# Performance work log

Hardware: AMD Instinct MI355X
Metric: run time of the kernel (lower is better)

The kernel has to match this reference:

```python
import jax, jax.numpy as jnp
import numpy as np

WS, OWS, HEADS, DIM = 16, 24, 6, 192
PAD = (OWS - WS) // 2
NQ, NKV = WS * WS, OWS * OWS
TABLE = (WS + OWS - 1) ** 2


def _rpi():
    # replicates WindowsHandling.get_relative_position_index_for_overlap_window
    c = np.arange(WS)
    ori = np.stack(np.meshgrid(c, c, indexing='ij')).reshape(2, -1)
    e = np.arange(OWS)
    ext = np.stack(np.meshgrid(e, e, indexing='ij')).reshape(2, -1)
    rc = (ext[:, None, :] - ori[:, :, None]).transpose(1, 2, 0).astype(np.int64)
    rc[..., 0] += WS - OWS + 1
    rc[..., 1] += WS - OWS + 1
    rc[..., 0] *= WS + OWS - 1
    # mod mimics torch's negative advanced-index wraparound into the table
    return (rc.sum(-1) % TABLE).astype(np.int32)  # (NQ, NKV)


def _extract_patches(xp, nh, nw):
    # torch.nn.Unfold(kernel=OWS, stride=WS) equivalent on NHWC input.
    # xp: (b, PH, PW, c) -> (b*nh*nw, OWS*OWS, c), row-major window order.
    b, PH, PW, c = xp.shape
    i = (np.arange(nh) * WS)[:, None] + np.arange(OWS)[None, :]
    j = (np.arange(nw) * WS)[:, None] + np.arange(OWS)[None, :]
    t = jnp.take(xp, jnp.asarray(i.reshape(-1)), axis=1).reshape(b, nh, OWS, PW, c)
    t = jnp.take(t, jnp.asarray(j.reshape(-1)), axis=3).reshape(b, nh, OWS, nw, OWS, c)
    return t.transpose(0, 1, 3, 2, 4, 5).reshape(b * nh * nw, OWS * OWS, c)


def _attn_mask(h, w):
    # shift_size == 0 branch of get_attention_mask_for_overlap_window:
    # kv positions falling into the zero padding get -100.
    vm = np.zeros((1, h + 2 * PAD, w + 2 * PAD, 1), np.float32)
    vm[:, PAD:-PAD, PAD:-PAD, :] = 1.0
    nh, nw = h // WS, w // WS
    kv = np.asarray(_extract_patches(jnp.asarray(vm), nh, nw)).reshape(nh * nw, NKV)
    m = np.where(kv[:, None, :] > 0, 0.0, -100.0).astype(np.float32)
    return np.broadcast_to(m, (nh * nw, NQ, NKV)).copy()


def setup_inputs():
    key = jax.random.key(0)
    ks = jax.random.split(key, 8)
    b, h, w = 2, 160, 160
    s = 0.02
    return {
        'x': jax.random.normal(ks[0], (b, h, w, DIM), jnp.float32),
        'rpi': jnp.asarray(_rpi()),
        'attn_mask': jnp.asarray(_attn_mask(h, w)),
        'q_w': jax.random.normal(ks[1], (DIM, DIM), jnp.float32) * s,
        'q_b': jnp.zeros((DIM,), jnp.float32),
        'kv_w': jax.random.normal(ks[2], (DIM, 2 * DIM), jnp.float32) * s,
        'kv_b': jnp.zeros((2 * DIM,), jnp.float32),
        'bias_table': jax.random.normal(ks[3], (TABLE, HEADS), jnp.float32) * s,
        'gating_w': jax.random.normal(ks[4], (DIM, DIM), jnp.float32) * s,
        'gating_b': jnp.ones((DIM,), jnp.float32),
        'proj_w': jax.random.normal(ks[5], (DIM, DIM), jnp.float32) * s,
        'proj_b': jnp.zeros((DIM,), jnp.float32),
    }


def reference(x, rpi, attn_mask, q_w, q_b, kv_w, kv_b, bias_table, gating_w, gating_b, proj_w, proj_b):
    b, h, w, c = x.shape
    d = c // HEADS
    scale = d ** -0.5
    nh, nw = h // WS, w // WS
    nwin = nh * nw
    # shift_size == 0 path: zero-pad for overlapping kv windows
    x_pad = jnp.pad(x, ((0, 0), (PAD, PAD), (PAD, PAD), (0, 0)))
    # q windows (non-overlapping window partition)
    xw = x.reshape(b, nh, WS, nw, WS, c).transpose(0, 1, 3, 2, 4, 5).reshape(b * nwin, NQ, c)
    # kv windows (overlapping, Unfold equivalent)
    xpw = _extract_patches(x_pad, nh, nw)  # (b*nwin, NKV, c)
    gates = xw @ gating_w + gating_b                       # (b*nwin, NQ, c)
    q = (xw @ q_w + q_b).reshape(-1, NQ, HEADS, d).transpose(0, 2, 1, 3) * scale
    kv = xpw @ kv_w + kv_b
    k = kv[..., :c].reshape(-1, NKV, HEADS, d).transpose(0, 2, 1, 3)
    v = kv[..., c:].reshape(-1, NKV, HEADS, d).transpose(0, 2, 1, 3)
    attn = jnp.einsum('bhqd,bhkd->bhqk', q, k)             # (b*nwin, H, NQ, NKV)
    bias = bias_table[rpi.reshape(-1)].reshape(NQ, NKV, HEADS).transpose(2, 0, 1)
    attn = attn + bias[None]
    attn = attn.reshape(b, nwin, HEADS, NQ, NKV) + attn_mask[None, :, None]
    attn = jax.nn.softmax(attn, axis=-1).reshape(b * nwin, HEADS, NQ, NKV)
    out = jnp.einsum('bhqk,bhkd->bhqd', attn, v).transpose(0, 2, 1, 3).reshape(-1, NQ, c)
    out = out * gates
    out = out.reshape(b, nh, nw, WS, WS, c).transpose(0, 1, 3, 2, 4, 5).reshape(b, h, w, c)
    return out @ proj_w + proj_b
```

## Files before the change

### kernel.cpp

```cpp
#include <hip/hip_runtime.h>
#include <hip/hip_bf16.h>
#include <stdint.h>

typedef __bf16 bf16x8  __attribute__((ext_vector_type(8)));
typedef __bf16 bf16x4  __attribute__((ext_vector_type(4)));
typedef __bf16 bf16x16 __attribute__((ext_vector_type(16)));
typedef float  f32x4   __attribute__((ext_vector_type(4)));
typedef float  f32x16  __attribute__((ext_vector_type(16)));
typedef uint32_t u32;

#define MFMA16(a, b, c) __builtin_amdgcn_mfma_f32_16x16x32_bf16((a), (b), (c), 0, 0, 0)
#define MFMA32(a, b, c) __builtin_amdgcn_mfma_f32_32x32x16_bf16((a), (b), (c), 0, 0, 0)

#if __has_builtin(__builtin_amdgcn_exp2f)
#define EXP2F(x) __builtin_amdgcn_exp2f(x)
#else
#define EXP2F(x) exp2f(x)
#endif

constexpr int CH = 160, CW = 160, CC = 192, CHEADS = 6, CD = 32;
constexpr int CNQ = 256, CNKV = 576, CPH = 168;
constexpr float LOG2E = 1.44269504088896340736f;
constexpr float QSCALE_L2E = 0.17677669529663687f * 1.44269504088896340736f;

__global__ __launch_bounds__(256)
void prep_k(const int* __restrict__ rpi, const float* __restrict__ tab,
            const float* __restrict__ q_w, const float* __restrict__ g_w,
            const float* __restrict__ kv_w, const float* __restrict__ p_w,
            const float* __restrict__ q_b, const float* __restrict__ g_b,
            const float* __restrict__ kv_b, const float* __restrict__ p_b,
            __bf16* __restrict__ BTh, u32* __restrict__ mt,
            __bf16* __restrict__ Wt, __bf16* __restrict__ Wp,
            float* __restrict__ b768, float* __restrict__ pb,
            __bf16* __restrict__ KVb)
{
    const int bidg = blockIdx.x;
    if (bidg < 216) {
        int idx = bidg * 256 + threadIdx.x;
        int lane = idx & 63;
        int rest = idx >> 6;
        int ktg = rest % 18; rest /= 18;
        int qtg = rest & 7;
        int head = rest >> 3;
        int l31 = lane & 31, hi = lane >> 5;
        int q = qtg * 32 + l31;
        bf16x16 o16;
#pragma unroll
        for (int g = 0; g < 4; ++g) {
            int4 ri = *(const int4*)(rpi + q * CNKV + ktg * 32 + 4 * hi + g * 8);
            o16[g * 4 + 0] = (__bf16)(tab[ri.x * CHEADS + head] * LOG2E);
            o16[g * 4 + 1] = (__bf16)(tab[ri.y * CHEADS + head] * LOG2E);
            o16[g * 4 + 2] = (__bf16)(tab[ri.z * CHEADS + head] * LOG2E);
            o16[g * 4 + 3] = (__bf16)(tab[ri.w * CHEADS + head] * LOG2E);
        }
        *(bf16x16*)(BTh + (long)idx * 16) = o16;
    } else if (bidg < 257) {
        int idx = (bidg - 216) * 256 + threadIdx.x;
        if (idx >= 9 * 18 * 64) return;
        int lane = idx & 63;
        int rest = idx >> 6;
        int ktg = rest % 18;
        int cls = rest / 18;
        int cy = cls / 3, cx = cls % 3;
        int hi = lane >> 5;
        u32 m = 0;
#pragma unroll
        for (int r = 0; r < 16; ++r) {
            int kv = ktg * 32 + 4 * hi + (r & 3) + 8 * (r >> 2);
            int oy = kv / 24, ox = kv - oy * 24;
            bool vy = (cy == 0) ? (oy >= 4) : ((cy == 2) ? (oy < 20) : true);
            bool vx = (cx == 0) ? (ox >= 4) : ((cx == 2) ? (ox < 20) : true);
            if (vy && vx) m |= (1u << r);
        }
        mt[idx] = m;
    } else if (bidg < 981) {
        int idx = (bidg - 257) * 256 + threadIdx.x;
        if (idx < 147456) {
            int n = idx / 192, k = idx - n * 192;
            float v;
            if (n < 192)      v = q_w[k * 192 + n] * QSCALE_L2E;
            else if (n < 384) v = g_w[k * 192 + (n - 192)];
            else              v = kv_w[k * 384 + (n - 384)];
            Wt[idx] = (__bf16)v;
        } else if (idx < 184320) {
            int j = idx - 147456;
            int n = j / 192, k = j - n * 192;
            Wp[j] = (__bf16)p_w[k * 192 + n];
        } else if (idx < 185280) {
            int j = idx - 184320;
            if (j < 192)      b768[j] = q_b[j] * QSCALE_L2E;
            else if (j < 384) b768[j] = g_b[j - 192];
            else if (j < 768) b768[j] = kv_b[j - 384];
            else              pb[j - 768] = p_b[j - 768];
        }
    } else {
        int tid = (bidg - 981) * 256 + threadIdx.x;
        if (tid >= 251904) return;
        int row = tid / 48, seg = tid - row * 48;
        int bb = row / 2624, rr = row - bb * 2624;
        int py, px;
        if (rr < 672)       { py = rr / 168;               px = rr % 168; }
        else if (rr < 1344) { int r2 = rr - 672; py = 164 + r2 / 168; px = r2 % 168; }
        else                { int rm = rr - 1344; py = 4 + rm / 8; int q = rm & 7;
                              px = (q < 4) ? q : 160 + q; }
        bf16x8 v;
#pragma unroll
        for (int j = 0; j < 8; ++j) v[j] = (__bf16)kv_b[seg * 8 + j];
        *(bf16x8*)(KVb + ((long)((bb * CPH + py) * CPH + px)) * 384 + seg * 8) = v;
    }
}

__global__ __launch_bounds__(256)
void gemm_f_k(const float* __restrict__ x, const __bf16* __restrict__ Wt,
              const float* __restrict__ b768,
              __bf16* __restrict__ Qb, __bf16* __restrict__ Gb,
              __bf16* __restrict__ KVb)
{
    __shared__ __bf16 As[2][4096];
    __shared__ __bf16 Bs[2][4096];

    const int bid = blockIdx.x;
    const int v = (bid & 7) * 1200 + (bid >> 3);
    const int bm = v / 12, bn = v - bm * 12;

    const int t = threadIdx.x, lane = t & 63, wv = t >> 6;
    const int l15 = lane & 15, l4 = lane >> 4;
    const int row = t >> 2, gp = t & 3;
    const int swz = row & 7;
    const int d0 = row * 64 + ((2 * gp) ^ swz) * 8;
    const int d1 = row * 64 + ((2 * gp + 1) ^ swz) * 8;

    const float*  asrc = x  + (long)(bm * 64 + row) * 192 + gp * 16;
    const __bf16* bsrc = Wt + (long)(bn * 64 + row) * 192 + gp * 16;

    float4 fa0, fa1, fa2, fa3;
    bf16x8 wb0, wb1;
    auto ld = [&](int kt) {
        const float* a = asrc + kt * 64;
        fa0 = ((const float4*)a)[0]; fa1 = ((const float4*)a)[1];
        fa2 = ((const float4*)a)[2]; fa3 = ((const float4*)a)[3];
        wb0 = *(const bf16x8*)(bsrc + kt * 64);
        wb1 = *(const bf16x8*)(bsrc + kt * 64 + 8);
    };
    auto st = [&](int buf) {
        bf16x8 g0, g1;
        g0[0] = (__bf16)fa0.x; g0[1] = (__bf16)fa0.y; g0[2] = (__bf16)fa0.z; g0[3] = (__bf16)fa0.w;
        g0[4] = (__bf16)fa1.x; g0[5] = (__bf16)fa1.y; g0[6] = (__bf16)fa1.z; g0[7] = (__bf16)fa1.w;
        g1[0] = (__bf16)fa2.x; g1[1] = (__bf16)fa2.y; g1[2] = (__bf16)fa2.z; g1[3] = (__bf16)fa2.w;
        g1[4] = (__bf16)fa3.x; g1[5] = (__bf16)fa3.y; g1[6] = (__bf16)fa3.z; g1[7] = (__bf16)fa3.w;
        *(bf16x8*)&As[buf][d0] = g0;
        *(bf16x8*)&As[buf][d1] = g1;
        *(bf16x8*)&Bs[buf][d0] = wb0;
        *(bf16x8*)&Bs[buf][d1] = wb1;
    };

    const int qm = (wv >> 1) * 32, qn = (wv & 1) * 32;
    f32x4 acc[2][2];
#pragma unroll
    for (int i = 0; i < 2; ++i)
#pragma unroll
        for (int j = 0; j < 2; ++j) acc[i][j] = f32x4{0.f, 0.f, 0.f, 0.f};

    ld(0);
    for (int kt = 0; kt < 3; ++kt) {
        const int buf = kt & 1;
        st(buf);
        if (kt < 2) ld(kt + 1);
        __syncthreads();
#pragma unroll
        for (int s = 0; s < 2; ++s) {
            bf16x8 af[2], bfr[2];
#pragma unroll
            for (int mi = 0; mi < 2; ++mi)
                af[mi] = *(const bf16x8*)&As[buf][(qm + mi * 16 + l15) * 64 +
                                                 (((s * 4 + l4) ^ (l15 & 7)) * 8)];
#pragma unroll
            for (int ni = 0; ni < 2; ++ni)
                bfr[ni] = *(const bf16x8*)&Bs[buf][(qn + ni * 16 + l15) * 64 +
                                                   (((s * 4 + l4) ^ (l15 & 7)) * 8)];
#pragma unroll
            for (int mi = 0; mi < 2; ++mi)
#pragma unroll
                for (int ni = 0; ni < 2; ++ni)
                    acc[mi][ni] = MFMA16(af[mi], bfr[ni], acc[mi][ni]);
        }
        __syncthreads();
    }

    __bf16* epi = &As[0][0];
    float bv0 = b768[bn * 64 + qn + l15];
    float bv1 = b768[bn * 64 + qn + 16 + l15];
#pragma unroll
    for (int mi = 0; mi < 2; ++mi)
#pragma unroll
        for (int ni = 0; ni < 2; ++ni)
#pragma unroll
            for (int r = 0; r < 4; ++r) {
                int rowl = qm + mi * 16 + l4 * 4 + r;
                int coll = qn + ni * 16 + l15;
                epi[rowl * 80 + coll] =
                    (__bf16)(acc[mi][ni][r] + (ni ? bv1 : bv0));
            }
    __syncthreads();
#pragma unroll
    for (int k = 0; k < 2; ++k) {
        int rid = t * 2 + k;
        int rowl = rid >> 3, seg = rid & 7;
        bf16x8 vv = *(const bf16x8*)&epi[rowl * 80 + seg * 8];
        int rowg = bm * 64 + rowl;
        int bb = rowg / 25600, rr = rowg - bb * 25600;
        int y = rr / 160, xx = rr - y * 160;
        int cg = bn * 64 + seg * 8;
        if (bn < 6) {
            int win = bb * 100 + (y >> 4) * 10 + (xx >> 4);
            long widx = ((long)win * 256 + (y & 15) * 16 + (xx & 15)) * 192;
            if (bn < 3) *(bf16x8*)(Qb + widx + cg) = vv;
            else        *(bf16x8*)(Gb + widx + cg - 192) = vv;
        } else {
            long kidx = ((long)((bb * CPH + y + 4) * CPH + (xx + 4))) * 384;
            *(bf16x8*)(KVb + kidx + cg - 384) = vv;
        }
    }
}

__global__ __launch_bounds__(256)
void gemm_p_k(const __bf16* __restrict__ Yb, const __bf16* __restrict__ Wp,
              const float* __restrict__ pb, float* __restrict__ of)
{
    __shared__ __bf16 As[2][4096];
    __shared__ __bf16 Bs[2][4096];

    const int bid = blockIdx.x;
    const int v = (bid & 7) * 300 + (bid >> 3);
    const int bm = v / 3, bn = v - bm * 3;

    const int t = threadIdx.x, lane = t & 63, wv = t >> 6;
    const int l15 = lane & 15, l4 = lane >> 4;
    const int row = t >> 2, gp = t & 3;
    const int swz = row & 7;
    const int d0 = row * 64 + ((2 * gp) ^ swz) * 8;
    const int d1 = row * 64 + ((2 * gp + 1) ^ swz) * 8;

    const __bf16* asrc = Yb + (long)(bm * 64 + row) * 192 + gp * 16;
    const __bf16* bsrc = Wp + (long)(bn * 64 + row) * 192 + gp * 16;

    bf16x8 a0, a1, wb0, wb1;
    auto ld = [&](int kt) {
        a0  = *(const bf16x8*)(asrc + kt * 64);
        a1  = *(const bf16x8*)(asrc + kt * 64 + 8);
        wb0 = *(const bf16x8*)(bsrc + kt * 64);
        wb1 = *(const bf16x8*)(bsrc + kt * 64 + 8);
    };
    auto st = [&](int buf) {
        *(bf16x8*)&As[buf][d0] = a0;
        *(bf16x8*)&As[buf][d1] = a1;
        *(bf16x8*)&Bs[buf][d0] = wb0;
        *(bf16x8*)&Bs[buf][d1] = wb1;
    };

    const int qm = (wv >> 1) * 32, qn = (wv & 1) * 32;
    f32x4 acc[2][2];
#pragma unroll
    for (int i = 0; i < 2; ++i)
#pragma unroll
        for (int j = 0; j < 2; ++j) acc[i][j] = f32x4{0.f, 0.f, 0.f, 0.f};

    ld(0);
    for (int kt = 0; kt < 3; ++kt) {
        const int buf = kt & 1;
        st(buf);
        if (kt < 2) ld(kt + 1);
        __syncthreads();
#pragma unroll
        for (int s = 0; s < 2; ++s) {
            bf16x8 af[2], bfr[2];
#pragma unroll
            for (int mi = 0; mi < 2; ++mi)
                af[mi] = *(const bf16x8*)&As[buf][(qm + mi * 16 + l15) * 64 +
                                                 (((s * 4 + l4) ^ (l15 & 7)) * 8)];
#pragma unroll
            for (int ni = 0; ni < 2; ++ni)
                bfr[ni] = *(const bf16x8*)&Bs[buf][(qn + ni * 16 + l15) * 64 +
                                                   (((s * 4 + l4) ^ (l15 & 7)) * 8)];
#pragma unroll
            for (int mi = 0; mi < 2; ++mi)
#pragma unroll
                for (int ni = 0; ni < 2; ++ni)
                    acc[mi][ni] = MFMA16(af[mi], bfr[ni], acc[mi][ni]);
        }
        __syncthreads();
    }

#pragma unroll
    for (int mi = 0; mi < 2; ++mi) {
#pragma unroll
        for (int r = 0; r < 4; ++r) {
            int rowg = bm * 64 + qm + mi * 16 + l4 * 4 + r;
            int win = rowg >> 8, q = rowg & 255;
            int bb = win / 100, wr = win % 100;
            int y = (wr / 10) * 16 + (q >> 4), xx = (wr % 10) * 16 + (q & 15);
            long oidx = ((long)((bb * CH + y) * CW + xx)) * 192;
#pragma unroll
            for (int ni = 0; ni < 2; ++ni) {
                int cg = bn * 64 + qn + ni * 16 + l15;
                of[oidx + cg] = acc[mi][ni][r] + pb[cg];
            }
        }
    }
}

__global__ __launch_bounds__(512, 4)
void attn14_k(const __bf16* __restrict__ Q, const __bf16* __restrict__ KV,
              const __bf16* __restrict__ G, const __bf16* __restrict__ BTh,
              const u32* __restrict__ MT, __bf16* __restrict__ Y)
{
    __shared__ __bf16 Ks[576][36];
    __shared__ __bf16 Vt[32][580];

    const int bid = blockIdx.x;
    const int xs = bid & 7, ii = bid >> 3;
    const int win = xs * 25 + ii / 6;
    const int head = ii % 6;

    const int bb = win / 100, wr = win % 100, wy = wr / 10, wx = wr % 10;
    const int cy = (wy == 0) ? 0 : ((wy == 9) ? 2 : 1);
    const int cx = (wx == 0) ? 0 : ((wx == 9) ? 2 : 1);
    const int cls = cy * 3 + cx;
    const int t = threadIdx.x, lane = t & 63, wv = t >> 6;
    const int l31 = lane & 31, hi = lane >> 5;

    {
        const int pos0 = t >> 3, seg = t & 7;
        int oy = pos0 / 24, ox = pos0 - oy * 24;
        const long rowbase = ((long)((bb * CPH + wy * 16) * CPH + wx * 16)) * 384
                             + head * CD;
        int pos = pos0;
#pragma unroll
        for (int r = 0; r < 9; ++r) {
            const __bf16* p = KV + rowbase + (long)(oy * CPH + ox) * 384;
            if (seg < 4) {
                bf16x8 k8 = *(const bf16x8*)(p + seg * 8);
                *(bf16x8*)&Ks[pos][seg * 8] = k8;
            } else {
                bf16x8 v8 = *(const bf16x8*)(p + 192 + (seg - 4) * 8);
#pragma unroll
                for (int j = 0; j < 8; ++j) Vt[(seg - 4) * 8 + j][pos] = v8[j];
            }
            pos += 64;
            oy += 2; ox += 16;
            if (ox >= 24) { ox -= 24; oy += 1; }
        }
    }

    bf16x8 qf0, qf1;
    {
        const __bf16* qb = Q + ((long)win * CNQ + wv * 32 + l31) * CC + head * CD;
        qf0 = *(const bf16x8*)(qb + hi * 8);
        qf1 = *(const bf16x8*)(qb + 16 + hi * 8);
    }
    const __bf16* btb = BTh + (long)((head * 8 + wv) * 18) * 1024 + (long)lane * 16;
    bf16x8 bA0 = *(const bf16x8*)(btb);
    bf16x8 bA1 = *(const bf16x8*)(btb + 8);

    bf16x8 ones8;
#pragma unroll
    for (int j = 0; j < 8; ++j) ones8[j] = (__bf16)1.0f;

    __syncthreads();

    f32x16 o = {};
    f32x16 sacc = {};

    const char* kbase = (const char*)&Ks[0][0] + l31 * 72 + hi * 16;
    const char* vbase = (const char*)&Vt[0][0] + l31 * 1160 + hi * 8;

    bf16x8 kc0 = *(const bf16x8*)(kbase);
    bf16x8 kc1 = *(const bf16x8*)(kbase + 32);

    for (int tt = 0; tt < 18; ++tt) {
        bf16x8 kn0, kn1, bB0, bB1;
        if (tt < 17) {
            const char* kn = kbase + (tt + 1) * 2304;
            kn0 = *(const bf16x8*)(kn);
            kn1 = *(const bf16x8*)(kn + 32);
            bB0 = *(const bf16x8*)(btb + (long)(tt + 1) * 1024);
            bB1 = *(const bf16x8*)(btb + (long)(tt + 1) * 1024 + 8);
        }

        const char* vp = vbase + tt * 64;
        bf16x4 v0 = *(const bf16x4*)(vp);
        bf16x4 v1 = *(const bf16x4*)(vp + 16);
        bf16x4 v2 = *(const bf16x4*)(vp + 32);
        bf16x4 v3 = *(const bf16x4*)(vp + 48);
        bf16x8 vf0, vf1;
#pragma unroll
        for (int j = 0; j < 4; ++j) {
            vf0[j] = v0[j]; vf0[4 + j] = v1[j];
            vf1[j] = v2[j]; vf1[4 + j] = v3[j];
        }

        f32x16 stv;
#pragma unroll
        for (int r = 0; r < 8; ++r) stv[r] = (float)bA0[r];
#pragma unroll
        for (int r = 0; r < 8; ++r) stv[8 + r] = (float)bA1[r];
        __builtin_amdgcn_s_setprio(1);
        stv = MFMA32(kc0, qf0, stv);
        stv = MFMA32(kc1, qf1, stv);
        __builtin_amdgcn_s_setprio(0);

        const bool needm = (cx != 1) || (cy == 0 && tt < 3) || (cy == 2 && tt >= 15);
        u32 m = 0xFFFFFFFFu;
        if (needm) m = MT[(cls * 18 + tt) * 64 + lane];

        float p[16];
#pragma unroll
        for (int r = 0; r < 16; ++r) p[r] = EXP2F(stv[r]);
        if (needm) {
#pragma unroll
            for (int r = 0; r < 16; ++r)
                p[r] = (m & (1u << r)) ? p[r] : 0.0f;
        }

        bf16x8 pa0, pa1;
#pragma unroll
        for (int j = 0; j < 8; ++j) {
            pa0[j] = (__bf16)p[j];
            pa1[j] = (__bf16)p[8 + j];
        }

        __builtin_amdgcn_s_setprio(1);
        o = MFMA32(vf0, pa0, o);
        o = MFMA32(vf1, pa1, o);
        sacc = MFMA32(ones8, pa0, sacc);
        sacc = MFMA32(ones8, pa1, sacc);
        __builtin_amdgcn_s_setprio(0);

        if (tt < 17) {
            asm volatile("" : "+v"(kn0), "+v"(kn1), "+v"(bB0), "+v"(bB1));
            kc0 = kn0; kc1 = kn1; bA0 = bB0; bA1 = bB1;
        }
    }

    float rs = 1.0f / sacc[0];
    long base = ((long)win * CNQ + wv * 32 + l31) * CC + head * CD;
    const __bf16* gp2 = G + base;
    __bf16* yp = Y + base;
#pragma unroll
    for (int g = 0; g < 4; ++g) {
        bf16x4 gv = *(const bf16x4*)(gp2 + g * 8 + 4 * hi);
        bf16x4 ov;
#pragma unroll
        for (int j = 0; j < 4; ++j)
            ov[j] = (__bf16)(o[g * 4 + j] * rs * (float)gv[j]);
        *(bf16x4*)(yp + g * 8 + 4 * hi) = ov;
    }
}

extern "C" void kernel_launch(void* const* d_in, const int* in_sizes, int n_in,
                              void* d_out, int out_size, void* d_ws, size_t ws_size,
                              hipStream_t stream)
{
    (void)in_sizes; (void)n_in; (void)out_size; (void)ws_size;
    const float* x    = (const float*)d_in[0];
    const int*   rpi  = (const int*)  d_in[1];
    const float* q_w  = (const float*)d_in[3];
    const float* q_b  = (const float*)d_in[4];
    const float* kv_w = (const float*)d_in[5];
    const float* kv_b = (const float*)d_in[6];
    const float* btab = (const float*)d_in[7];
    const float* g_w  = (const float*)d_in[8];
    const float* g_b  = (const float*)d_in[9];
    const float* p_w  = (const float*)d_in[10];
    const float* p_b  = (const float*)d_in[11];
    float* out = (float*)d_out;

    char* ws = (char*)d_ws;
    __bf16* Qb  = (__bf16*)(ws);
    __bf16* KVb = (__bf16*)(ws + 19660800);
    __bf16* Gb  = (__bf16*)(ws + 63012864);
    __bf16* Yb  = (__bf16*)(ws + 82673664);
    __bf16* BTh = (__bf16*)(ws + 102334464);
    u32*    MT  = (u32*)   (ws + 104103936);
    __bf16* Wt  = (__bf16*)(ws + 104145408);
    __bf16* Wp  = (__bf16*)(ws + 104440320);
    float*  b768= (float*) (ws + 104514048);
    float*  pb  = (float*) (ws + 104517120);

    prep_k<<<1965, 256, 0, stream>>>(rpi, btab, q_w, g_w, kv_w, p_w,
                                     q_b, g_b, kv_b, p_b,
                                     BTh, MT, Wt, Wp, b768, pb, KVb);
    gemm_f_k<<<9600, 256, 0, stream>>>(x, Wt, b768, Qb, Gb, KVb);
    attn14_k<<<1200, 512, 0, stream>>>(Qb, KVb, Gb, BTh, MT, Yb);
    gemm_p_k<<<2400, 256, 0, stream>>>(Yb, Wp, pb, out);
}
```

Before: 139.9 us.

## Load full K=192 tiles into LDS once in both GEMMs, dropping double buffering

Both the input-projection GEMM and the output-projection GEMM now stage the whole 64x192 A and B tiles into shared memory in one pass, then run six unrolled MFMA steps after a single barrier. This replaces the three-stage register-prefetch/double-buffer loop and its per-stage barriers. The cost is more LDS per block (48KB vs 32KB), which may lower occupancy, and load latency is no longer hidden behind compute. Separately, an empty asm register constraint in the attention kernel's K/bias prefetch handoff is removed, which frees the compiler to reschedule those moves.

```diff
diff --git a/kernel.cpp b/kernel.cpp
--- a/kernel.cpp
+++ b/kernel.cpp
@@ -116,8 +116,8 @@
               __bf16* __restrict__ Qb, __bf16* __restrict__ Gb,
               __bf16* __restrict__ KVb)
 {
-    __shared__ __bf16 As[2][4096];
-    __shared__ __bf16 Bs[2][4096];
+    __shared__ __bf16 As[64 * 192];
+    __shared__ __bf16 Bs[64 * 192];
 
     const int bid = blockIdx.x;
     const int v = (bid & 7) * 1200 + (bid >> 3);
@@ -127,32 +127,32 @@
     const int l15 = lane & 15, l4 = lane >> 4;
     const int row = t >> 2, gp = t & 3;
     const int swz = row & 7;
-    const int d0 = row * 64 + ((2 * gp) ^ swz) * 8;
-    const int d1 = row * 64 + ((2 * gp + 1) ^ swz) * 8;
-
-    const float*  asrc = x  + (long)(bm * 64 + row) * 192 + gp * 16;
-    const __bf16* bsrc = Wt + (long)(bn * 64 + row) * 192 + gp * 16;
-
-    float4 fa0, fa1, fa2, fa3;
-    bf16x8 wb0, wb1;
-    auto ld = [&](int kt) {
-        const float* a = asrc + kt * 64;
-        fa0 = ((const float4*)a)[0]; fa1 = ((const float4*)a)[1];
-        fa2 = ((const float4*)a)[2]; fa3 = ((const float4*)a)[3];
-        wb0 = *(const bf16x8*)(bsrc + kt * 64);
-        wb1 = *(const bf16x8*)(bsrc + kt * 64 + 8);
-    };
-    auto st = [&](int buf) {
-        bf16x8 g0, g1;
-        g0[0] = (__bf16)fa0.x; g0[1] = (__bf16)fa0.y; g0[2] = (__bf16)fa0.z; g0[3] = (__bf16)fa0.w;
-        g0[4] = (__bf16)fa1.x; g0[5] = (__bf16)fa1.y; g0[6] = (__bf16)fa1.z; g0[7] = (__bf16)fa1.w;
-        g1[0] = (__bf16)fa2.x; g1[1] = (__bf16)fa2.y; g1[2] = (__bf16)fa2.z; g1[3] = (__bf16)fa2.w;
-        g1[4] = (__bf16)fa3.x; g1[5] = (__bf16)fa3.y; g1[6] = (__bf16)fa3.z; g1[7] = (__bf16)fa3.w;
-        *(bf16x8*)&As[buf][d0] = g0;
-        *(bf16x8*)&As[buf][d1] = g1;
-        *(bf16x8*)&Bs[buf][d0] = wb0;
-        *(bf16x8*)&Bs[buf][d1] = wb1;
-    };
+
+    {
+        const float*  asrc = x  + (long)(bm * 64 + row) * 192;
+        const __bf16* bsrc = Wt + (long)(bn * 64 + row) * 192;
+#pragma unroll
+        for (int c = 0; c < 3; ++c) {
+            const int col = c * 64 + gp * 16;
+            float4 q0 = ((const float4*)(asrc + col))[0];
+            float4 q1 = ((const float4*)(asrc + col))[1];
+            float4 q2 = ((const float4*)(asrc + col))[2];
+            float4 q3 = ((const float4*)(asrc + col))[3];
+            bf16x8 g0, g1;
+            g0[0] = (__bf16)q0.x; g0[1] = (__bf16)q0.y; g0[2] = (__bf16)q0.z; g0[3] = (__bf16)q0.w;
+            g0[4] = (__bf16)q1.x; g0[5] = (__bf16)q1.y; g0[6] = (__bf16)q1.z; g0[7] = (__bf16)q1.w;
+            g1[0] = (__bf16)q2.x; g1[1] = (__bf16)q2.y; g1[2] = (__bf16)q2.z; g1[3] = (__bf16)q2.w;
+            g1[4] = (__bf16)q3.x; g1[5] = (__bf16)q3.y; g1[6] = (__bf16)q3.z; g1[7] = (__bf16)q3.w;
+            const int grp = c * 8 + gp * 2;
+            *(bf16x8*)&As[row * 192 + (grp ^ swz) * 8] = g0;
+            *(bf16x8*)&As[row * 192 + ((grp + 1) ^ swz) * 8] = g1;
+            bf16x8 w0 = *(const bf16x8*)(bsrc + col);
+            bf16x8 w1 = *(const bf16x8*)(bsrc + col + 8);
+            *(bf16x8*)&Bs[row * 192 + (grp ^ swz) * 8] = w0;
+            *(bf16x8*)&Bs[row * 192 + ((grp + 1) ^ swz) * 8] = w1;
+        }
+    }
+    __syncthreads();
 
     const int qm = (wv >> 1) * 32, qn = (wv & 1) * 32;
     f32x4 acc[2][2];
@@ -161,33 +161,26 @@
 #pragma unroll
         for (int j = 0; j < 2; ++j) acc[i][j] = f32x4{0.f, 0.f, 0.f, 0.f};
 
-    ld(0);
-    for (int kt = 0; kt < 3; ++kt) {
-        const int buf = kt & 1;
-        st(buf);
-        if (kt < 2) ld(kt + 1);
-        __syncthreads();
-#pragma unroll
-        for (int s = 0; s < 2; ++s) {
-            bf16x8 af[2], bfr[2];
-#pragma unroll
-            for (int mi = 0; mi < 2; ++mi)
-                af[mi] = *(const bf16x8*)&As[buf][(qm + mi * 16 + l15) * 64 +
-                                                 (((s * 4 + l4) ^ (l15 & 7)) * 8)];
+#pragma unroll
+    for (int step = 0; step < 6; ++step) {
+        bf16x8 af[2], bfr[2];
+#pragma unroll
+        for (int mi = 0; mi < 2; ++mi)
+            af[mi] = *(const bf16x8*)&As[(qm + mi * 16 + l15) * 192 +
+                                        (((step * 4 + l4) ^ (l15 & 7)) * 8)];
+#pragma unroll
+        for (int ni = 0; ni < 2; ++ni)
+            bfr[ni] = *(const bf16x8*)&Bs[(qn + ni * 16 + l15) * 192 +
+                                          (((step * 4 + l4) ^ (l15 & 7)) * 8)];
+#pragma unroll
+        for (int mi = 0; mi < 2; ++mi)
 #pragma unroll
             for (int ni = 0; ni < 2; ++ni)
-                bfr[ni] = *(const bf16x8*)&Bs[buf][(qn + ni * 16 + l15) * 64 +
-                                                   (((s * 4 + l4) ^ (l15 & 7)) * 8)];
-#pragma unroll
-            for (int mi = 0; mi < 2; ++mi)
-#pragma unroll
-                for (int ni = 0; ni < 2; ++ni)
-                    acc[mi][ni] = MFMA16(af[mi], bfr[ni], acc[mi][ni]);
-        }
-        __syncthreads();
-    }
-
-    __bf16* epi = &As[0][0];
+                acc[mi][ni] = MFMA16(af[mi], bfr[ni], acc[mi][ni]);
+    }
+    __syncthreads();
+
+    __bf16* epi = &As[0];
     float bv0 = b768[bn * 64 + qn + l15];
     float bv1 = b768[bn * 64 + qn + 16 + l15];
 #pragma unroll
@@ -227,8 +220,8 @@
 void gemm_p_k(const __bf16* __restrict__ Yb, const __bf16* __restrict__ Wp,
               const float* __restrict__ pb, float* __restrict__ of)
 {
-    __shared__ __bf16 As[2][4096];
-    __shared__ __bf16 Bs[2][4096];
+    __shared__ __bf16 As[64 * 192];
+    __shared__ __bf16 Bs[64 * 192];
 
     const int bid = blockIdx.x;
     const int v = (bid & 7) * 300 + (bid >> 3);
@@ -238,25 +231,25 @@
     const int l15 = lane & 15, l4 = lane >> 4;
     const int row = t >> 2, gp = t & 3;
     const int swz = row & 7;
-    const int d0 = row * 64 + ((2 * gp) ^ swz) * 8;
-    const int d1 = row * 64 + ((2 * gp + 1) ^ swz) * 8;
-
-    const __bf16* asrc = Yb + (long)(bm * 64 + row) * 192 + gp * 16;
-    const __bf16* bsrc = Wp + (long)(bn * 64 + row) * 192 + gp * 16;
-
-    bf16x8 a0, a1, wb0, wb1;
-    auto ld = [&](int kt) {
-        a0  = *(const bf16x8*)(asrc + kt * 64);
-        a1  = *(const bf16x8*)(asrc + kt * 64 + 8);
-        wb0 = *(const bf16x8*)(bsrc + kt * 64);
-        wb1 = *(const bf16x8*)(bsrc + kt * 64 + 8);
-    };
-    auto st = [&](int buf) {
-        *(bf16x8*)&As[buf][d0] = a0;
-        *(bf16x8*)&As[buf][d1] = a1;
-        *(bf16x8*)&Bs[buf][d0] = wb0;
-        *(bf16x8*)&Bs[buf][d1] = wb1;
-    };
+
+    {
+        const __bf16* asrc = Yb + (long)(bm * 64 + row) * 192;
+        const __bf16* bsrc = Wp + (long)(bn * 64 + row) * 192;
+#pragma unroll
+        for (int c = 0; c < 3; ++c) {
+            const int col = c * 64 + gp * 16;
+            const int grp = c * 8 + gp * 2;
+            bf16x8 a0 = *(const bf16x8*)(asrc + col);
+            bf16x8 a1 = *(const bf16x8*)(asrc + col + 8);
+            *(bf16x8*)&As[row * 192 + (grp ^ swz) * 8] = a0;
+            *(bf16x8*)&As[row * 192 + ((grp + 1) ^ swz) * 8] = a1;
+            bf16x8 w0 = *(const bf16x8*)(bsrc + col);
+            bf16x8 w1 = *(const bf16x8*)(bsrc + col + 8);
+            *(bf16x8*)&Bs[row * 192 + (grp ^ swz) * 8] = w0;
+            *(bf16x8*)&Bs[row * 192 + ((grp + 1) ^ swz) * 8] = w1;
+        }
+    }
+    __syncthreads();
 
     const int qm = (wv >> 1) * 32, qn = (wv & 1) * 32;
     f32x4 acc[2][2];
@@ -265,30 +258,22 @@
 #pragma unroll
         for (int j = 0; j < 2; ++j) acc[i][j] = f32x4{0.f, 0.f, 0.f, 0.f};
 
-    ld(0);
-    for (int kt = 0; kt < 3; ++kt) {
-        const int buf = kt & 1;
-        st(buf);
-        if (kt < 2) ld(kt + 1);
-        __syncthreads();
-#pragma unroll
-        for (int s = 0; s < 2; ++s) {
-            bf16x8 af[2], bfr[2];
-#pragma unroll
-            for (int mi = 0; mi < 2; ++mi)
-                af[mi] = *(const bf16x8*)&As[buf][(qm + mi * 16 + l15) * 64 +
-                                                 (((s * 4 + l4) ^ (l15 & 7)) * 8)];
+#pragma unroll
+    for (int step = 0; step < 6; ++step) {
+        bf16x8 af[2], bfr[2];
+#pragma unroll
+        for (int mi = 0; mi < 2; ++mi)
+            af[mi] = *(const bf16x8*)&As[(qm + mi * 16 + l15) * 192 +
+                                        (((step * 4 + l4) ^ (l15 & 7)) * 8)];
+#pragma unroll
+        for (int ni = 0; ni < 2; ++ni)
+            bfr[ni] = *(const bf16x8*)&Bs[(qn + ni * 16 + l15) * 192 +
+                                          (((step * 4 + l4) ^ (l15 & 7)) * 8)];
+#pragma unroll
+        for (int mi = 0; mi < 2; ++mi)
 #pragma unroll
             for (int ni = 0; ni < 2; ++ni)
-                bfr[ni] = *(const bf16x8*)&Bs[buf][(qn + ni * 16 + l15) * 64 +
-                                                   (((s * 4 + l4) ^ (l15 & 7)) * 8)];
-#pragma unroll
-            for (int mi = 0; mi < 2; ++mi)
-#pragma unroll
-                for (int ni = 0; ni < 2; ++ni)
-                    acc[mi][ni] = MFMA16(af[mi], bfr[ni], acc[mi][ni]);
-        }
-        __syncthreads();
+                acc[mi][ni] = MFMA16(af[mi], bfr[ni], acc[mi][ni]);
     }
 
 #pragma unroll
@@ -437,7 +422,6 @@
         __builtin_amdgcn_s_setprio(0);
 
         if (tt < 17) {
-            asm volatile("" : "+v"(kn0), "+v"(kn1), "+v"(bB0), "+v"(bB1));
             kc0 = kn0; kc1 = kn1; bA0 = bB0; bA1 = bB1;
         }
     }
```

Result: no change. 141.7 us (+1.2%).

## Swizzle V layout, inject bias via identity MFMA, compute rpi analytically

Applied to the files above, without the earlier changes.

The attention kernel now stores transposed V with a permuted column order so each lane fetches its V fragment with two 16-byte LDS loads instead of four 8-byte loads and a repack. It also adds the relative-position bias through two extra MFMAs against a per-lane identity fragment, replacing the per-element bf16-to-float unpack into the accumulator, and matching the bias table layout to that fragment. The prep kernel computes relative position indices arithmetically instead of reading the rpi array. The trade-off is two extra MFMAs per tile and removal of the register-pinning asm barrier, which may change scheduling.

```diff
diff --git a/kernel.cpp b/kernel.cpp
--- a/kernel.cpp
+++ b/kernel.cpp
@@ -34,6 +34,7 @@
             float* __restrict__ b768, float* __restrict__ pb,
             __bf16* __restrict__ KVb)
 {
+    (void)rpi;
     const int bidg = blockIdx.x;
     if (bidg < 216) {
         int idx = bidg * 256 + threadIdx.x;
@@ -43,15 +44,17 @@
         int qtg = rest & 7;
         int head = rest >> 3;
         int l31 = lane & 31, hi = lane >> 5;
-        int q = qtg * 32 + l31;
+        int kv = ktg * 32 + l31;
+        int oy = kv / 24, ox = kv - oy * 24;
         bf16x16 o16;
 #pragma unroll
-        for (int g = 0; g < 4; ++g) {
-            int4 ri = *(const int4*)(rpi + q * CNKV + ktg * 32 + 4 * hi + g * 8);
-            o16[g * 4 + 0] = (__bf16)(tab[ri.x * CHEADS + head] * LOG2E);
-            o16[g * 4 + 1] = (__bf16)(tab[ri.y * CHEADS + head] * LOG2E);
-            o16[g * 4 + 2] = (__bf16)(tab[ri.z * CHEADS + head] * LOG2E);
-            o16[g * 4 + 3] = (__bf16)(tab[ri.w * CHEADS + head] * LOG2E);
+        for (int e = 0; e < 16; ++e) {
+            int h = e >> 3, j = e & 7;
+            int q = qtg * 32 + h * 16 + hi * 8 + j;
+            int qy = q >> 4, qx = q & 15;
+            int ri = 39 * (oy - qy - 7) + (ox - qx - 7);
+            if (ri < 0) ri += 1521;
+            o16[e] = (__bf16)(tab[ri * CHEADS + head] * LOG2E);
         }
         *(bf16x16*)(BTh + (long)idx * 16) = o16;
     } else if (bidg < 257) {
@@ -310,12 +313,12 @@
 }
 
 __global__ __launch_bounds__(512, 4)
-void attn14_k(const __bf16* __restrict__ Q, const __bf16* __restrict__ KV,
+void attn15_k(const __bf16* __restrict__ Q, const __bf16* __restrict__ KV,
               const __bf16* __restrict__ G, const __bf16* __restrict__ BTh,
               const u32* __restrict__ MT, __bf16* __restrict__ Y)
 {
     __shared__ __bf16 Ks[576][36];
-    __shared__ __bf16 Vt[32][580];
+    __shared__ __bf16 Vt[32][584];
 
     const int bid = blockIdx.x;
     const int xs = bid & 7, ii = bid >> 3;
@@ -343,8 +346,10 @@
                 *(bf16x8*)&Ks[pos][seg * 8] = k8;
             } else {
                 bf16x8 v8 = *(const bf16x8*)(p + 192 + (seg - 4) * 8);
-#pragma unroll
-                for (int j = 0; j < 8; ++j) Vt[(seg - 4) * 8 + j][pos] = v8[j];
+                int w = pos & 31;
+                int cp = (pos & ~31) | (w & 19) | ((w & 4) << 1) | ((w & 8) >> 1);
+#pragma unroll
+                for (int j = 0; j < 8; ++j) Vt[(seg - 4) * 8 + j][cp] = v8[j];
             }
             pos += 64;
             oy += 2; ox += 16;
@@ -362,9 +367,13 @@
     bf16x8 bA0 = *(const bf16x8*)(btb);
     bf16x8 bA1 = *(const bf16x8*)(btb + 8);
 
-    bf16x8 ones8;
-#pragma unroll
-    for (int j = 0; j < 8; ++j) ones8[j] = (__bf16)1.0f;
+    bf16x8 ones8, I0, I1;
+#pragma unroll
+    for (int j = 0; j < 8; ++j) {
+        ones8[j] = (__bf16)1.0f;
+        I0[j] = (__bf16)((l31 == hi * 8 + j) ? 1.0f : 0.0f);
+        I1[j] = (__bf16)((l31 == 16 + hi * 8 + j) ? 1.0f : 0.0f);
+    }
 
     __syncthreads();
 
@@ -372,7 +381,7 @@
     f32x16 sacc = {};
 
     const char* kbase = (const char*)&Ks[0][0] + l31 * 72 + hi * 16;
-    const char* vbase = (const char*)&Vt[0][0] + l31 * 1160 + hi * 8;
+    const char* vbase = (const char*)&Vt[0][0] + l31 * 1168 + hi * 16;
 
     bf16x8 kc0 = *(const bf16x8*)(kbase);
     bf16x8 kc1 = *(const bf16x8*)(kbase + 32);
@@ -388,23 +397,13 @@
         }
 
         const char* vp = vbase + tt * 64;
-        bf16x4 v0 = *(const bf16x4*)(vp);
-        bf16x4 v1 = *(const bf16x4*)(vp + 16);
-        bf16x4 v2 = *(const bf16x4*)(vp + 32);
-        bf16x4 v3 = *(const bf16x4*)(vp + 48);
-        bf16x8 vf0, vf1;
-#pragma unroll
-        for (int j = 0; j < 4; ++j) {
-            vf0[j] = v0[j]; vf0[4 + j] = v1[j];
-            vf1[j] = v2[j]; vf1[4 + j] = v3[j];
-        }
-
-        f32x16 stv;
-#pragma unroll
-        for (int r = 0; r < 8; ++r) stv[r] = (float)bA0[r];
-#pragma unroll
-        for (int r = 0; r < 8; ++r) stv[8 + r] = (float)bA1[r];
+        bf16x8 vf0 = *(const bf16x8*)(vp);
+        bf16x8 vf1 = *(const bf16x8*)(vp + 32);
+
+        f32x16 stv = {};
         __builtin_amdgcn_s_setprio(1);
+        stv = MFMA32(bA0, I0, stv);
+        stv = MFMA32(bA1, I1, stv);
         stv = MFMA32(kc0, qf0, stv);
         stv = MFMA32(kc1, qf1, stv);
         __builtin_amdgcn_s_setprio(0);
@@ -437,7 +436,6 @@
         __builtin_amdgcn_s_setprio(0);
 
         if (tt < 17) {
-            asm volatile("" : "+v"(kn0), "+v"(kn1), "+v"(bB0), "+v"(bB1));
             kc0 = kn0; kc1 = kn1; bA0 = bB0; bA1 = bB1;
         }
     }
@@ -491,6 +489,6 @@
                                      q_b, g_b, kv_b, p_b,
                                      BTh, MT, Wt, Wp, b768, pb, KVb);
     gemm_f_k<<<9600, 256, 0, stream>>>(x, Wt, b768, Qb, Gb, KVb);
-    attn14_k<<<1200, 512, 0, stream>>>(Qb, KVb, Gb, BTh, MT, Yb);
+    attn15_k<<<1200, 512, 0, stream>>>(Qb, KVb, Gb, BTh, MT, Yb);
     gemm_p_k<<<2400, 256, 0, stream>>>(Yb, Wp, pb, out);
 }
```

New measurement: 138.9 us. About the same (-0.8%).
